# Kernel tuning notes

Measured on AMD Instinct MI355X. Metric: run time of the kernel, lower is better.

Reference implementation:

```python
import jax, jax.numpy as jnp
import numpy as np

B, S, H, V = 64, 256, 1024, 10000


def setup_inputs() -> dict:
    key = jax.random.key(0)
    ks = jax.random.split(key, 16)
    s = 1.0 / np.sqrt(H)
    return {
        "input_seq": jax.random.randint(ks[0], (B,), 0, V),
        "last_hidden": jax.random.normal(ks[1], (1, 1, H), jnp.float32),
        "encoder_outputs": jax.random.normal(ks[2], (S, B, H), jnp.float32),
        "emb_table": jax.random.normal(ks[3], (V, H), jnp.float32) * s,
        "W_ih": jax.random.normal(ks[4], (3 * H, H), jnp.float32) * s,
        "W_hh": jax.random.normal(ks[5], (3 * H, H), jnp.float32) * s,
        "b_ih": jax.random.normal(ks[6], (3 * H,), jnp.float32) * s,
        "b_hh": jax.random.normal(ks[7], (3 * H,), jnp.float32) * s,
        "W_attn": jax.random.normal(ks[8], (H, 2 * H), jnp.float32) * s,
        "b_attn": jax.random.normal(ks[9], (H,), jnp.float32) * s,
        "v_attn": jax.random.normal(ks[10], (H,), jnp.float32) * s,
        "W_concat": jax.random.normal(ks[11], (H, 2 * H), jnp.float32) * s,
        "b_concat": jax.random.normal(ks[12], (H,), jnp.float32) * s,
        "W_out": jax.random.normal(ks[13], (V, H), jnp.float32) * s,
        "b_out": jax.random.normal(ks[14], (V,), jnp.float32) * s,
    }


def _gru_scan(x_seq, h0, W_ih, W_hh, b_ih, b_hh):
    # x_seq: [T, H] (here T == batch dim, per the module's batch_first quirk)
    def step(h, x):
        gi = x @ W_ih.T + b_ih   # [3H]
        gh = h @ W_hh.T + b_hh   # [3H]
        ir, iz, inn = jnp.split(gi, 3)
        hr, hz, hn = jnp.split(gh, 3)
        r = jax.nn.sigmoid(ir + hr)
        z = jax.nn.sigmoid(iz + hz)
        n = jnp.tanh(inn + r * hn)
        h_new = (1.0 - z) * n + z * h
        return h_new, h_new

    h_last, outs = jax.lax.scan(step, h0, x_seq)
    return outs, h_last


def reference(input_seq, last_hidden, encoder_outputs, emb_table, W_ih, W_hh,
              b_ih, b_hh, W_attn, b_attn, v_attn, W_concat, b_concat, W_out, b_out):
    embedded = emb_table[input_seq]                       # [B, H]
    # GRU fed [1, B, H] with batch_first=True -> recurs over B with one hidden
    rnn_output, h_last = _gru_scan(embedded, last_hidden[0, 0], W_ih, W_hh, b_ih, b_hh)
    hidden = h_last[None, None, :]                        # [1, 1, H]

    # concat attention: score(b,i) = v . (W_attn @ [h_b ; enc_ib] + b_attn)
    enc = jnp.transpose(encoder_outputs, (1, 0, 2))       # [B, S, H]
    h_bc = jnp.broadcast_to(rnn_output[:, None, :], (B, S, H))
    cat = jnp.concatenate([h_bc, enc], axis=-1)           # [B, S, 2H]
    energy = jnp.einsum('bsk,hk->bsh', cat, W_attn) + b_attn
    scores = jnp.einsum('bsh,h->bs', energy, v_attn)      # [B, S]
    attn_weights = jax.nn.softmax(scores, axis=-1)[:, None, :]  # [B, 1, S]

    context = jnp.einsum('bs,bsh->bh', attn_weights[:, 0, :], enc)  # [B, H]
    concat_input = jnp.concatenate([rnn_output, context], axis=-1)  # [B, 2H]
    concat_output = jnp.tanh(concat_input @ W_concat.T + b_concat)  # [B, H]
    output = concat_output @ W_out.T + b_out                        # [B, V]
    return output, hidden, attn_weights
```

## Files before the change

### kernel.cpp

```cpp
#include <hip/hip_runtime.h>
#include <math.h>

#define kH  1024
#define kB  64
#define kS  256
#define kV  10000
#define kH3 3072

__device__ __forceinline__ float warp_sum(float v) {
#pragma unroll
  for (int off = 32; off > 0; off >>= 1) v += __shfl_down(v, off, 64);
  return v;
}
__device__ __forceinline__ float warp_max_all(float v) {
#pragma unroll
  for (int off = 32; off > 0; off >>= 1) v = fmaxf(v, __shfl_xor(v, off, 64));
  return v;
}
__device__ __forceinline__ float warp_sum_all(float v) {
#pragma unroll
  for (int off = 32; off > 0; off >>= 1) v += __shfl_xor(v, off, 64);
  return v;
}
__device__ __forceinline__ float sigmoidf_(float x) {
  return __fdividef(1.0f, 1.0f + __expf(-x));
}
__device__ __forceinline__ float tanhf_(float x) {
  const float t = __expf(-2.0f * fabsf(x));
  const float r = __fdividef(1.0f - t, 1.0f + t);
  return copysignf(r, x);
}

__global__ __launch_bounds__(256) void k_gi(const int* __restrict__ seq,
    const float* __restrict__ emb, const float* __restrict__ W_ih,
    const float* __restrict__ b_ih, float* __restrict__ GI) {
  const int lane = threadIdx.x & 63;
  const int r = blockIdx.x * 4 + (threadIdx.x >> 6);
  const float4* wp = (const float4*)(W_ih + (size_t)r * kH) + lane * 4;
  const float4 w0 = wp[0], w1 = wp[1], w2 = wp[2], w3 = wp[3];
  const float br = b_ih[r];
  for (int t = 0; t < kB; ++t) {
    const int tok = seq[t];
    const float4* xp = (const float4*)(emb + (size_t)tok * kH) + lane * 4;
    const float4 x0 = xp[0], x1 = xp[1], x2 = xp[2], x3 = xp[3];
    float acc = w0.x*x0.x + w0.y*x0.y + w0.z*x0.z + w0.w*x0.w;
    acc += w1.x*x1.x + w1.y*x1.y + w1.z*x1.z + w1.w*x1.w;
    acc += w2.x*x2.x + w2.y*x2.y + w2.z*x2.z + w2.w*x2.w;
    acc += w3.x*x3.x + w3.y*x3.y + w3.z*x3.z + w3.w*x3.w;
    acc = warp_sum(acc);
    if (lane == 0) GI[(size_t)t * kH3 + r] = acc + br;
  }
}

__global__ __launch_bounds__(1024, 4) void k_gru(const float* __restrict__ h0,
    const float* __restrict__ W_hh, const float* __restrict__ b_hh,
    const float* __restrict__ GI, float* __restrict__ rnn,
    unsigned long long* __restrict__ step) {
  __shared__ float hs[2][kH];
  const int tid  = threadIdx.x;
  const int lane = tid & 63;
  const int w    = tid >> 6;
  const int bid  = blockIdx.x;
  const int j    = bid * 16 + w;

  float wv[3][16];
#pragma unroll
  for (int q = 0; q < 3; ++q) {
    const float* base = W_hh + ((size_t)q * kH + j) * kH + lane;
#pragma unroll
    for (int u = 0; u < 16; ++u) wv[q][u] = base[u * 64];
  }
#pragma unroll
  for (int q = 0; q < 3; ++q)
#pragma unroll
    for (int u = 0; u < 16; ++u)
      asm volatile("" : "+v"(wv[q][u]));

  const float bhr = b_hh[j];
  const float bhz = b_hh[kH + j];
  const float bhn = b_hh[2 * kH + j];

  for (int t = 0; t < kB; ++t) {
    float gir = GI[(size_t)t * kH3 + j];
    float giz = GI[(size_t)t * kH3 + kH + j];
    float gin = GI[(size_t)t * kH3 + 2 * kH + j];
    asm volatile("" :: "v"(gir), "v"(giz), "v"(gin));

    float* hb = hs[t & 1];
    if (t == 0) {
      hb[tid] = h0[tid];
    } else {
      const unsigned long long* sb = step + (size_t)(t - 1) * kH;
      const unsigned want = (unsigned)t;
      float v0;
      while (true) {
        const unsigned long long x = __hip_atomic_load(&sb[tid],
            __ATOMIC_RELAXED, __HIP_MEMORY_SCOPE_AGENT);
        if ((unsigned)(x >> 32) == want) { v0 = __uint_as_float((unsigned)x); break; }
        __builtin_amdgcn_s_sleep(1);
      }
      hb[tid] = v0;
    }
    __syncthreads();

    float hx[16];
#pragma unroll
    for (int u = 0; u < 16; ++u) hx[u] = hb[u * 64 + lane];

    float d[3];
#pragma unroll
    for (int q = 0; q < 3; ++q) {
      float acc = 0.f;
#pragma unroll
      for (int u = 0; u < 16; ++u) acc += wv[q][u] * hx[u];
      d[q] = acc;
    }
#pragma unroll
    for (int q = 0; q < 3; ++q) d[q] = warp_sum(d[q]);

    if (lane == 0) {
      const float ho = hb[j];
      const float r = sigmoidf_(gir + d[0] + bhr);
      const float z = sigmoidf_(giz + d[1] + bhz);
      const float n = tanhf_(gin + r * (d[2] + bhn));
      const float hn = (1.f - z) * n + z * ho;
      rnn[(size_t)t * kH + j] = hn;
      __hip_atomic_store(&step[(size_t)t * kH + j],
                         (((unsigned long long)(t + 1)) << 32) | __float_as_uint(hn),
                         __ATOMIC_RELAXED, __HIP_MEMORY_SCOPE_AGENT);
    }
  }
}

__global__ __launch_bounds__(256) void k_w2h(const float* __restrict__ W_attn,
    const float* __restrict__ v_attn, float* __restrict__ w2h) {
  __shared__ float4 red[256];
  const int t  = threadIdx.x;
  const int k0 = kH + blockIdx.x * 4;
  float ax = 0, ay = 0, az = 0, aw = 0;
  for (int h = t; h < kH; h += 256) {
    const float vh = v_attn[h];
    const float4 wq = *(const float4*)(W_attn + (size_t)h * 2048 + k0);
    ax += vh * wq.x; ay += vh * wq.y; az += vh * wq.z; aw += vh * wq.w;
  }
  red[t] = make_float4(ax, ay, az, aw);
  __syncthreads();
  for (int s = 128; s > 0; s >>= 1) {
    if (t < s) {
      const float4 a = red[t], b = red[t + s];
      red[t] = make_float4(a.x + b.x, a.y + b.y, a.z + b.z, a.w + b.w);
    }
    __syncthreads();
  }
  if (t == 0) *(float4*)(w2h + blockIdx.x * 4) = red[0];
}

__global__ __launch_bounds__(256) void k_scores(const float* __restrict__ enc,
    const float* __restrict__ w2h, float* __restrict__ sc) {
  const int lane = threadIdx.x & 63;
  const int wg = blockIdx.x * 4 + (threadIdx.x >> 6);
  const int b = wg & 63, s = wg >> 6;
  const float4* ep = (const float4*)(enc + ((size_t)s * kB + b) * kH) + lane * 4;
  const float4* wp = (const float4*)w2h + lane * 4;
  float acc = 0.f;
#pragma unroll
  for (int c = 0; c < 4; ++c) {
    const float4 e = ep[c], wq = wp[c];
    acc += e.x * wq.x + e.y * wq.y + e.z * wq.z + e.w * wq.w;
  }
  acc = warp_sum(acc);
  if (lane == 0) sc[b * kS + s] = acc;
}

__global__ __launch_bounds__(256) void k_softmax(const float* __restrict__ sc,
                                                 float* __restrict__ attn) {
  __shared__ float sm[4], ss[4];
  const int b = blockIdx.x, t = threadIdx.x, lane = t & 63, w = t >> 6;
  const float x = sc[b * kS + t];
  float m = warp_max_all(x);
  if (lane == 0) sm[w] = m;
  __syncthreads();
  m = fmaxf(fmaxf(sm[0], sm[1]), fmaxf(sm[2], sm[3]));
  const float e = __expf(x - m);
  float s = warp_sum_all(e);
  if (lane == 0) ss[w] = s;
  __syncthreads();
  s = ss[0] + ss[1] + ss[2] + ss[3];
  attn[b * kS + t] = e / s;
}

__global__ __launch_bounds__(256) void k_context(const float* __restrict__ enc,
    const float* __restrict__ attn, float* __restrict__ part) {
  const int b  = blockIdx.x & 63;
  const int ch = blockIdx.x >> 6;
  const int h0 = threadIdx.x * 4;
  float ax = 0, ay = 0, az = 0, aw = 0;
  const int s0 = ch * 64;
#pragma unroll 4
  for (int s = s0; s < s0 + 64; ++s) {
    const float a = attn[b * kS + s];
    const float4 v = *(const float4*)(enc + ((size_t)s * kB + b) * kH + h0);
    ax += a * v.x; ay += a * v.y; az += a * v.z; aw += a * v.w;
  }
  *(float4*)(part + ((size_t)ch * kB + b) * kH + h0) =
      make_float4(ax, ay, az, aw);
}

__global__ __launch_bounds__(256) void k_ctxsum(const float* __restrict__ part,
    const float* __restrict__ rnn, float* __restrict__ ctx,
    float* __restrict__ hid) {
  const int b = blockIdx.x;
  const int h0 = threadIdx.x * 4;
  float4 s = *(const float4*)(part + ((size_t)0 * kB + b) * kH + h0);
#pragma unroll
  for (int c = 1; c < 4; ++c) {
    const float4 p = *(const float4*)(part + ((size_t)c * kB + b) * kH + h0);
    s.x += p.x; s.y += p.y; s.z += p.z; s.w += p.w;
  }
  *(float4*)(ctx + (size_t)b * kH + h0) = s;
  if (b < 4) {
    const int i = b * 256 + threadIdx.x;
    hid[i] = rnn[63 * kH + i];
  }
}

__global__ __launch_bounds__(256) void k_concat(const float* __restrict__ rnn,
    const float* __restrict__ ctx, const float* __restrict__ W_c,
    const float* __restrict__ b_c, float* __restrict__ coT) {
  const int lane = threadIdx.x & 63;
  const int iq = blockIdx.x >> 2;
  const int bq = blockIdx.x & 3;
  const int i  = iq * 4 + (threadIdx.x >> 6);
  float wreg[32];
  {
    const float4* wp = (const float4*)(W_c + (size_t)i * 2048) + lane * 8;
#pragma unroll
    for (int c = 0; c < 8; ++c) {
      const float4 f = wp[c];
      wreg[c * 4 + 0] = f.x; wreg[c * 4 + 1] = f.y;
      wreg[c * 4 + 2] = f.z; wreg[c * 4 + 3] = f.w;
    }
  }
  const float bc = b_c[i];
  const int jcol = lane * 32;
  const float* xbase = (jcol < kH) ? (rnn + jcol) : (ctx + (jcol - kH));
  for (int b = bq * 16; b < bq * 16 + 16; ++b) {
    const float* xr = xbase + (size_t)b * kH;
    float acc = 0.f;
#pragma unroll
    for (int c = 0; c < 8; ++c) {
      const float4 x = *(const float4*)(xr + c * 4);
      acc += wreg[c * 4 + 0] * x.x + wreg[c * 4 + 1] * x.y +
             wreg[c * 4 + 2] * x.z + wreg[c * 4 + 3] * x.w;
    }
    acc = warp_sum(acc);
    if (lane == 0) coT[(size_t)i * kB + b] = tanhf(acc + bc);
  }
}

__global__ __launch_bounds__(256) void k_out(const float* __restrict__ coT,
    const float* __restrict__ W_out, const float* __restrict__ b_out,
    float* __restrict__ out) {
  __shared__ float wlds[16 * kH];
  const int v0 = blockIdx.x * 16;
  {
    const float4* src = (const float4*)(W_out + (size_t)v0 * kH);
    float4 tmp[16];
#pragma unroll
    for (int c = 0; c < 16; ++c) tmp[c] = src[threadIdx.x + 256 * c];
    float4* dst = (float4*)wlds;
#pragma unroll
    for (int c = 0; c < 16; ++c) dst[threadIdx.x + 256 * c] = tmp[c];
  }
  __syncthreads();

  const int lane = threadIdx.x & 63;
  const int w    = threadIdx.x >> 6;
  float acc[4] = {0.f, 0.f, 0.f, 0.f};
#pragma unroll 2
  for (int h = 0; h < kH; h += 4) {
    const float x0 = coT[(size_t)(h + 0) * kB + lane];
    const float x1 = coT[(size_t)(h + 1) * kB + lane];
    const float x2 = coT[(size_t)(h + 2) * kB + lane];
    const float x3 = coT[(size_t)(h + 3) * kB + lane];
#pragma unroll
    for (int vi = 0; vi < 4; ++vi) {
      const float4 wq = *(const float4*)&wlds[(w * 4 + vi) * kH + h];
      acc[vi] += wq.x * x0 + wq.y * x1 + wq.z * x2 + wq.w * x3;
    }
  }
  const float4 bq = *(const float4*)(b_out + v0 + w * 4);
  float4 r;
  r.x = acc[0] + bq.x; r.y = acc[1] + bq.y;
  r.z = acc[2] + bq.z; r.w = acc[3] + bq.w;
  *(float4*)&out[(size_t)lane * kV + v0 + w * 4] = r;
}

extern "C" void kernel_launch(void* const* d_in, const int* in_sizes, int n_in,
                              void* d_out, int out_size, void* d_ws,
                              size_t ws_size, hipStream_t stream) {
  const int*   seq    = (const int*)  d_in[0];
  const float* h0     = (const float*)d_in[1];
  const float* enc    = (const float*)d_in[2];
  const float* emb    = (const float*)d_in[3];
  const float* W_ih   = (const float*)d_in[4];
  const float* W_hh   = (const float*)d_in[5];
  const float* b_ih   = (const float*)d_in[6];
  const float* b_hh   = (const float*)d_in[7];
  const float* W_attn = (const float*)d_in[8];
  const float* v_attn = (const float*)d_in[10];
  const float* W_conc = (const float*)d_in[11];
  const float* b_conc = (const float*)d_in[12];
  const float* W_outp = (const float*)d_in[13];
  const float* b_outp = (const float*)d_in[14];

  float* out      = (float*)d_out;
  float* out_hid  = out + 640000;
  float* out_attn = out + 641024;

  float* ws = (float*)d_ws;
  float* GI   = ws;
  float* RNN  = ws + 196608;
  unsigned long long* STEP =
      (unsigned long long*)(ws + 262144);
  float* W2H  = ws + 393216;
  float* SC   = ws + 394240;
  float* PART = ws + 410624;
  float* CTX  = ws + 672768;
  float* COT  = ws + 738304;

  k_gi<<<768, 256, 0, stream>>>(seq, emb, W_ih, b_ih, GI);
  k_gru<<<64, 1024, 0, stream>>>(h0, W_hh, b_hh, GI, RNN, STEP);
  k_w2h<<<256, 256, 0, stream>>>(W_attn, v_attn, W2H);
  k_scores<<<4096, 256, 0, stream>>>(enc, W2H, SC);
  k_softmax<<<64, 256, 0, stream>>>(SC, out_attn);
  k_context<<<256, 256, 0, stream>>>(enc, out_attn, PART);
  k_ctxsum<<<64, 256, 0, stream>>>(PART, RNN, CTX, out_hid);
  k_concat<<<1024, 256, 0, stream>>>(RNN, CTX, W_conc, b_conc, COT);
  k_out<<<625, 256, 0, stream>>>(COT, W_outp, b_outp, out);
}
```

Measured before the change: 610.0 us.

## Spread GRU over 256 blocks with LDS weights; fuse softmax and context kernels

The persistent GRU kernel moves from 64 blocks of 1024 threads holding W_hh in registers to 256 blocks of 256 threads that hold their 12 weight rows in LDS. Each thread now polls four hidden-state flags per step, and the h vector is read as float4. This spreads the recurrence over more CUs, at the cost of more blocks taking part in the cross-block spin synchronisation. Separately, the softmax, context partial and context-sum kernels are fused into one 1024-thread kernel per batch row, which removes two launches and the partial-sum round trip through global memory.

```diff
diff --git a/kernel.cpp b/kernel.cpp
--- a/kernel.cpp
+++ b/kernel.cpp
@@ -52,29 +52,26 @@
   }
 }
 
-__global__ __launch_bounds__(1024, 4) void k_gru(const float* __restrict__ h0,
+__global__ __launch_bounds__(256) void k_gru(const float* __restrict__ h0,
     const float* __restrict__ W_hh, const float* __restrict__ b_hh,
     const float* __restrict__ GI, float* __restrict__ rnn,
     unsigned long long* __restrict__ step) {
-  __shared__ float hs[2][kH];
+  __shared__ float4 wlds4[12 * 256];
+  __shared__ __align__(16) float hs[2][kH];
   const int tid  = threadIdx.x;
   const int lane = tid & 63;
   const int w    = tid >> 6;
   const int bid  = blockIdx.x;
-  const int j    = bid * 16 + w;
-
-  float wv[3][16];
-#pragma unroll
-  for (int q = 0; q < 3; ++q) {
-    const float* base = W_hh + ((size_t)q * kH + j) * kH + lane;
-#pragma unroll
-    for (int u = 0; u < 16; ++u) wv[q][u] = base[u * 64];
-  }
-#pragma unroll
-  for (int q = 0; q < 3; ++q)
-#pragma unroll
-    for (int u = 0; u < 16; ++u)
-      asm volatile("" : "+v"(wv[q][u]));
+  const int j    = bid * 4 + w;
+
+#pragma unroll
+  for (int c = 0; c < 12; ++c) {
+    const int f    = c * 256 + tid;
+    const int row  = f >> 8;
+    const int col4 = f & 255;
+    const int q    = row >> 2, r = row & 3;
+    wlds4[f] = ((const float4*)(W_hh + ((size_t)q * kH + bid * 4 + r) * kH))[col4];
+  }
 
   const float bhr = b_hh[j];
   const float bhz = b_hh[kH + j];
@@ -88,31 +85,50 @@
 
     float* hb = hs[t & 1];
     if (t == 0) {
-      hb[tid] = h0[tid];
+      ((float4*)hb)[tid] = ((const float4*)h0)[tid];
     } else {
       const unsigned long long* sb = step + (size_t)(t - 1) * kH;
       const unsigned want = (unsigned)t;
-      float v0;
+      const int i0 = tid * 4;
+      bool done[4] = {false, false, false, false};
+      float v[4];
       while (true) {
-        const unsigned long long x = __hip_atomic_load(&sb[tid],
-            __ATOMIC_RELAXED, __HIP_MEMORY_SCOPE_AGENT);
-        if ((unsigned)(x >> 32) == want) { v0 = __uint_as_float((unsigned)x); break; }
+        bool all = true;
+#pragma unroll
+        for (int k = 0; k < 4; ++k) {
+          if (!done[k]) {
+            const unsigned long long x = __hip_atomic_load(&sb[i0 + k],
+                __ATOMIC_RELAXED, __HIP_MEMORY_SCOPE_AGENT);
+            if ((unsigned)(x >> 32) == want) {
+              v[k] = __uint_as_float((unsigned)x);
+              done[k] = true;
+            } else {
+              all = false;
+            }
+          }
+        }
+        if (all) break;
         __builtin_amdgcn_s_sleep(1);
       }
-      hb[tid] = v0;
+#pragma unroll
+      for (int k = 0; k < 4; ++k) hb[i0 + k] = v[k];
     }
     __syncthreads();
 
-    float hx[16];
-#pragma unroll
-    for (int u = 0; u < 16; ++u) hx[u] = hb[u * 64 + lane];
+    float4 hx4[4];
+#pragma unroll
+    for (int c = 0; c < 4; ++c) hx4[c] = ((const float4*)hb)[lane + 64 * c];
 
     float d[3];
 #pragma unroll
     for (int q = 0; q < 3; ++q) {
       float acc = 0.f;
 #pragma unroll
-      for (int u = 0; u < 16; ++u) acc += wv[q][u] * hx[u];
+      for (int c = 0; c < 4; ++c) {
+        const float4 wq = wlds4[(q * 4 + w) * 256 + lane + 64 * c];
+        const float4 h4 = hx4[c];
+        acc += wq.x * h4.x + wq.y * h4.y + wq.z * h4.z + wq.w * h4.w;
+      }
       d[q] = acc;
     }
 #pragma unroll
@@ -172,55 +188,63 @@
   if (lane == 0) sc[b * kS + s] = acc;
 }
 
-__global__ __launch_bounds__(256) void k_softmax(const float* __restrict__ sc,
-                                                 float* __restrict__ attn) {
+__global__ __launch_bounds__(1024) void k_ctx2(const float* __restrict__ sc,
+    const float* __restrict__ enc, const float* __restrict__ rnn,
+    float* __restrict__ attn, float* __restrict__ ctx,
+    float* __restrict__ hid) {
+  __shared__ float aw[kS];
   __shared__ float sm[4], ss[4];
-  const int b = blockIdx.x, t = threadIdx.x, lane = t & 63, w = t >> 6;
-  const float x = sc[b * kS + t];
-  float m = warp_max_all(x);
-  if (lane == 0) sm[w] = m;
-  __syncthreads();
-  m = fmaxf(fmaxf(sm[0], sm[1]), fmaxf(sm[2], sm[3]));
-  const float e = __expf(x - m);
-  float s = warp_sum_all(e);
-  if (lane == 0) ss[w] = s;
-  __syncthreads();
-  s = ss[0] + ss[1] + ss[2] + ss[3];
-  attn[b * kS + t] = e / s;
-}
-
-__global__ __launch_bounds__(256) void k_context(const float* __restrict__ enc,
-    const float* __restrict__ attn, float* __restrict__ part) {
-  const int b  = blockIdx.x & 63;
-  const int ch = blockIdx.x >> 6;
-  const int h0 = threadIdx.x * 4;
-  float ax = 0, ay = 0, az = 0, aw = 0;
-  const int s0 = ch * 64;
+  __shared__ float4 part4[1024];
+  const int b = blockIdx.x, tid = threadIdx.x;
+  const int lane = tid & 63, w = tid >> 6;
+
+  float x = 0.f, e = 0.f;
+  if (tid < kS) {
+    x = sc[b * kS + tid];
+    const float m = warp_max_all(x);
+    if (lane == 0) sm[w] = m;
+  }
+  __syncthreads();
+  if (tid < kS) {
+    const float m = fmaxf(fmaxf(sm[0], sm[1]), fmaxf(sm[2], sm[3]));
+    e = __expf(x - m);
+    const float s = warp_sum_all(e);
+    if (lane == 0) ss[w] = s;
+  }
+  __syncthreads();
+  if (tid < kS) {
+    const float s = ss[0] + ss[1] + ss[2] + ss[3];
+    const float a = e / s;
+    attn[b * kS + tid] = a;
+    aw[tid] = a;
+  }
+  if (b < 4 && tid < kS) {
+    hid[b * kS + tid] = rnn[63 * kH + b * kS + tid];
+  }
+  __syncthreads();
+
+  const int hc = tid & 255;
+  const int sq = tid >> 8;
+  const float4* encb = (const float4*)enc;
+  float4 acc = make_float4(0.f, 0.f, 0.f, 0.f);
+  const int s0 = sq * 64;
 #pragma unroll 4
   for (int s = s0; s < s0 + 64; ++s) {
-    const float a = attn[b * kS + s];
-    const float4 v = *(const float4*)(enc + ((size_t)s * kB + b) * kH + h0);
-    ax += a * v.x; ay += a * v.y; az += a * v.z; aw += a * v.w;
-  }
-  *(float4*)(part + ((size_t)ch * kB + b) * kH + h0) =
-      make_float4(ax, ay, az, aw);
-}
-
-__global__ __launch_bounds__(256) void k_ctxsum(const float* __restrict__ part,
-    const float* __restrict__ rnn, float* __restrict__ ctx,
-    float* __restrict__ hid) {
-  const int b = blockIdx.x;
-  const int h0 = threadIdx.x * 4;
-  float4 s = *(const float4*)(part + ((size_t)0 * kB + b) * kH + h0);
-#pragma unroll
-  for (int c = 1; c < 4; ++c) {
-    const float4 p = *(const float4*)(part + ((size_t)c * kB + b) * kH + h0);
-    s.x += p.x; s.y += p.y; s.z += p.z; s.w += p.w;
-  }
-  *(float4*)(ctx + (size_t)b * kH + h0) = s;
-  if (b < 4) {
-    const int i = b * 256 + threadIdx.x;
-    hid[i] = rnn[63 * kH + i];
+    const float a = aw[s];
+    const float4 v = encb[((size_t)s * kB + b) * 256 + hc];
+    acc.x += a * v.x; acc.y += a * v.y; acc.z += a * v.z; acc.w += a * v.w;
+  }
+  part4[tid] = acc;
+  __syncthreads();
+  if (tid < 256) {
+    const float4 p0 = part4[tid], p1 = part4[tid + 256];
+    const float4 p2 = part4[tid + 512], p3 = part4[tid + 768];
+    float4 r;
+    r.x = p0.x + p1.x + p2.x + p3.x;
+    r.y = p0.y + p1.y + p2.y + p3.y;
+    r.z = p0.z + p1.z + p2.z + p3.z;
+    r.w = p0.w + p1.w + p2.w + p3.w;
+    ((float4*)(ctx + (size_t)b * kH))[tid] = r;
   }
 }
 
@@ -325,17 +349,14 @@
       (unsigned long long*)(ws + 262144);
   float* W2H  = ws + 393216;
   float* SC   = ws + 394240;
-  float* PART = ws + 410624;
   float* CTX  = ws + 672768;
   float* COT  = ws + 738304;
 
   k_gi<<<768, 256, 0, stream>>>(seq, emb, W_ih, b_ih, GI);
-  k_gru<<<64, 1024, 0, stream>>>(h0, W_hh, b_hh, GI, RNN, STEP);
+  k_gru<<<256, 256, 0, stream>>>(h0, W_hh, b_hh, GI, RNN, STEP);
   k_w2h<<<256, 256, 0, stream>>>(W_attn, v_attn, W2H);
   k_scores<<<4096, 256, 0, stream>>>(enc, W2H, SC);
-  k_softmax<<<64, 256, 0, stream>>>(SC, out_attn);
-  k_context<<<256, 256, 0, stream>>>(enc, out_attn, PART);
-  k_ctxsum<<<64, 256, 0, stream>>>(PART, RNN, CTX, out_hid);
+  k_ctx2<<<64, 1024, 0, stream>>>(SC, enc, RNN, out_attn, CTX, out_hid);
   k_concat<<<1024, 256, 0, stream>>>(RNN, CTX, W_conc, b_conc, COT);
   k_out<<<625, 256, 0, stream>>>(COT, W_outp, b_outp, out);
 }
```

New measurement: 539.2 us. -11.6%, faster.
